# Kernel tuning notes

Hardware: AMD Instinct MI355X
Metric: run time of the kernel (lower is better)

## Reference

```python
import jax, jax.numpy as jnp
import numpy as np

NUM_HEADS = 12
D = 768
HD = D // NUM_HEADS  # 64

def setup_inputs() -> dict:
    key = jax.random.key(0)
    ks = jax.random.split(key, 9)
    s = 0.02
    return {
        "x": jax.random.normal(ks[0], (4, 2048, D), dtype=jnp.float32),
        "QW_w": jax.random.normal(ks[1], (D, D), dtype=jnp.float32) * s,
        "QW_b": jax.random.normal(ks[2], (D,), dtype=jnp.float32) * s,
        "KW_w": jax.random.normal(ks[3], (D, D), dtype=jnp.float32) * s,
        "KW_b": jax.random.normal(ks[4], (D,), dtype=jnp.float32) * s,
        "VW_w": jax.random.normal(ks[5], (D, D), dtype=jnp.float32) * s,
        "VW_b": jax.random.normal(ks[6], (D,), dtype=jnp.float32) * s,
        "OW_w": jax.random.normal(ks[7], (D, D), dtype=jnp.float32) * s,
        "OW_b": jax.random.normal(ks[8], (D,), dtype=jnp.float32) * s,
    }

def reference(x, QW_w, QW_b, KW_w, KW_b, VW_w, VW_b, OW_w, OW_b):
    b, s, _ = x.shape
    # torch nn.Linear: y = x @ W.T + b
    def proj(w, bias):
        y = jnp.einsum('bsd,ed->bse', x, w) + bias
        return y.reshape(b, s, NUM_HEADS, HD).transpose(0, 2, 1, 3)  # [b,h,s,hd]
    q = proj(QW_w, QW_b)
    k = proj(KW_w, KW_b)
    v = proj(VW_w, VW_b)
    scores = jnp.einsum('bhqd,bhkd->bhqk', q, k) / jnp.sqrt(jnp.float32(HD))
    attn = jax.nn.softmax(scores, axis=-1)
    out = jnp.einsum('bhqk,bhkd->bhqd', attn, v)
    out = out.transpose(0, 2, 1, 3).reshape(b, s, NUM_HEADS * HD)
    return jnp.einsum('bsd,ed->bse', out, OW_w) + OW_b
```

## Files before the change

kernel.cpp:

```cpp
#include <hip/hip_runtime.h>
#include <hip/hip_bf16.h>

#define NH  12
#define HD  64
#define DIM 768
#define SEQ 2048
#define NB  4
#define MM  (NB*SEQ)
#define NKB (SEQ/64)
#define N4X (MM*DIM/4)
#define N4W (DIM*DIM/4)

typedef short    v8s  __attribute__((ext_vector_type(8)));
typedef float    v4f  __attribute__((ext_vector_type(4)));
typedef float    v16f __attribute__((ext_vector_type(16)));
typedef unsigned v4u  __attribute__((ext_vector_type(4)));

#if __has_builtin(__builtin_amdgcn_exp2f)
#define EXP2(x) __builtin_amdgcn_exp2f(x)
#else
#define EXP2(x) __builtin_exp2f(x)
#endif

static __device__ __forceinline__ unsigned short f2b(float f) {
    unsigned int u = __float_as_uint(f);
    return (unsigned short)((u + 0x7FFFu + ((u >> 16) & 1u)) >> 16);
}
static __device__ __forceinline__ unsigned cvtpk(float lo, float hi) {
    unsigned r;
    asm("v_cvt_pk_bf16_f32 %0, %1, %2" : "=v"(r) : "v"(lo), "v"(hi));
    return r;
}
static __device__ __forceinline__ void g2l16(const unsigned short* g, unsigned short* l) {
    __builtin_amdgcn_global_load_lds(
        (const __attribute__((address_space(1))) void*)g,
        (__attribute__((address_space(3))) void*)l, 16, 0, 0);
}

__global__ void cast_all(const float* __restrict__ x,
                         const float* __restrict__ qw, const float* __restrict__ kw,
                         const float* __restrict__ vw, const float* __restrict__ ow,
                         unsigned short* __restrict__ xb,
                         unsigned short* __restrict__ wqb, unsigned short* __restrict__ wkb,
                         unsigned short* __restrict__ wvb, unsigned short* __restrict__ wob)
{
    int i = blockIdx.x * blockDim.x + threadIdx.x;
    const float* in; unsigned short* out; int idx;
    if (i < N4X) {
        in = x; out = xb; idx = i;
    } else {
        int j = i - N4X;
        int s = j / N4W;
        idx = j - s * N4W;
        switch (s) {
            case 0:  in = qw; out = wqb; break;
            case 1:  in = kw; out = wkb; break;
            case 2:  in = vw; out = wvb; break;
            default: in = ow; out = wob; break;
        }
    }
    float4 v = reinterpret_cast<const float4*>(in)[idx];
    ushort4 o;
    o.x = f2b(v.x); o.y = f2b(v.y); o.z = f2b(v.z); o.w = f2b(v.w);
    reinterpret_cast<ushort4*>(out)[idx] = o;
}

__global__ __launch_bounds__(256, 3) void gemm_qkv(
    const unsigned short* __restrict__ A,
    const unsigned short* __restrict__ Wq,
    const unsigned short* __restrict__ Wk,
    const unsigned short* __restrict__ Wv,
    const float* __restrict__ bq,
    const float* __restrict__ bk,
    const float* __restrict__ bvp,
    unsigned short* __restrict__ Qb,
    unsigned short* __restrict__ Kfo,
    unsigned short* __restrict__ Vf)
{
    __shared__ __align__(16) unsigned short As[128 * 64];
    __shared__ __align__(16) unsigned short Bs[3][64 * 64];

    const int tid  = threadIdx.x;
    const int w    = tid >> 6, lane = tid & 63;
    const int quad = lane >> 4, l16 = lane & 15;
    const int wm   = w & 1,  wn = w >> 1;
    const int lane8 = lane >> 3, sc = lane & 7;
    const int m0   = blockIdx.x * 128;
    const int h    = blockIdx.y;
    const int n0   = h * 64;

    v4f acc[3][4][2];
    #pragma unroll
    for (int s = 0; s < 3; ++s)
        #pragma unroll
        for (int i = 0; i < 4; ++i)
            #pragma unroll
            for (int j = 0; j < 2; ++j)
                acc[s][i][j] = v4f{0.f, 0.f, 0.f, 0.f};

    for (int kb = 0; kb < DIM; kb += 64) {
        __syncthreads();
        #pragma unroll
        for (int t = 0; t < 4; ++t) {
            int r8 = w * 32 + t * 8;
            int r  = r8 + lane8;
            int gch = sc ^ (r & 7);
            g2l16(&A[(size_t)(m0 + r) * DIM + kb + gch * 8], &As[r8 * 64]);
        }
        #pragma unroll
        for (int u = 0; u < 6; ++u) {
            int G = w * 6 + u;
            int set = G >> 3, rg = G & 7;
            int row = rg * 8 + lane8;
            int gch = sc ^ (row & 7);
            const unsigned short* Wp = (set == 0) ? Wq : (set == 1) ? Wk : Wv;
            g2l16(&Wp[(size_t)(n0 + row) * DIM + kb + gch * 8], &Bs[set][rg * 8 * 64]);
        }
        __syncthreads();
        #pragma unroll
        for (int kk = 0; kk < 64; kk += 32) {
            int chb = kk >> 3;
            v8s a[4];
            #pragma unroll
            for (int i = 0; i < 4; ++i) {
                int m = wm * 64 + i * 16 + l16;
                a[i] = *reinterpret_cast<const v8s*>(
                    &As[m * 64 + (((chb + quad) ^ (m & 7)) << 3)]);
            }
            #pragma unroll
            for (int s = 0; s < 3; ++s) {
                v8s b[2];
                #pragma unroll
                for (int j = 0; j < 2; ++j) {
                    int n = wn * 32 + j * 16 + l16;
                    b[j] = *reinterpret_cast<const v8s*>(
                        &Bs[s][n * 64 + (((chb + quad) ^ (n & 7)) << 3)]);
                }
                #pragma unroll
                for (int i = 0; i < 4; ++i)
                    #pragma unroll
                    for (int j = 0; j < 2; ++j)
                        acc[s][i][j] = __builtin_amdgcn_mfma_f32_16x16x32_bf16(
                            a[i], b[j], acc[s][i][j], 0, 0, 0);
            }
        }
    }

    #pragma unroll
    for (int i = 0; i < 4; ++i) {
        #pragma unroll
        for (int j = 0; j < 2; ++j) {
            int hd = wn * 32 + j * 16 + l16;
            float bias_v = bq[n0 + hd];
            #pragma unroll
            for (int r = 0; r < 4; ++r) {
                int gm = m0 + wm * 64 + i * 16 + quad * 4 + r;
                int bb = gm >> 11, sq = gm & (SEQ - 1);
                Qb[((size_t)(bb * NH + h) * SEQ + sq) * HD + hd] =
                    f2b((acc[0][i][j][r] + bias_v) * 0.1803368801f);
            }
        }
    }
    #pragma unroll
    for (int i = 0; i < 4; ++i) {
        int kh = i >> 1;
        #pragma unroll
        for (int j = 0; j < 2; ++j) {
            int hd = wn * 32 + j * 16 + l16;
            int c  = hd >> 4;
            int half_a = (l16 >> 3) & 1;
            int jj = l16 & 7;
            float bias_v = bk[n0 + hd];
            int gm0 = m0 + wm * 64 + i * 16 + quad * 4;
            int bb = gm0 >> 11, sk = gm0 & (SEQ - 1);
            int t = sk >> 6;
            int l31k = (i & 1) * 16 + quad * 4;
            size_t frag = ((size_t)(bb * NH + h) * NKB + t) * 8 + kh * 4 + c;
            unsigned short* dst = &Kfo[frag * 512 + (half_a * 32 + l31k) * 8 + jj];
            #pragma unroll
            for (int r = 0; r < 4; ++r)
                dst[r * 8] = f2b(acc[1][i][j][r] + bias_v);
        }
    }
    #pragma unroll
    for (int i = 0; i < 4; ++i) {
        #pragma unroll
        for (int j = 0; j < 2; ++j) {
            int hd = wn * 32 + j * 16 + l16;
            int hb = hd >> 5, l31v = hd & 31;
            float bias_v = bvp[n0 + hd];
            int gm0 = m0 + wm * 64 + i * 16 + quad * 4;
            int bb = gm0 >> 11, sk = gm0 & (SEQ - 1);
            int kbi = sk >> 6;
            int halfv = quad >> 1, j0 = (quad & 1) * 4;
            ushort4 pkv;
            pkv.x = f2b(acc[2][i][j][0] + bias_v);
            pkv.y = f2b(acc[2][i][j][1] + bias_v);
            pkv.z = f2b(acc[2][i][j][2] + bias_v);
            pkv.w = f2b(acc[2][i][j][3] + bias_v);
            size_t frag = ((size_t)(bb * NH + h) * NKB + kbi) * 8 + hb * 4 + i;
            *reinterpret_cast<ushort4*>(
                &Vf[frag * 512 + (halfv * 32 + l31v) * 8 + j0]) = pkv;
        }
    }
}

__global__ __launch_bounds__(256, 3) void gemm_o(
    const unsigned short* __restrict__ A,
    const unsigned short* __restrict__ W,
    const float* __restrict__ bias,
    float* __restrict__ out)
{
    __shared__ __align__(16) unsigned short As[128 * 64];
    __shared__ __align__(16) unsigned short Bs[64 * 64];

    const int tid  = threadIdx.x;
    const int w    = tid >> 6, lane = tid & 63;
    const int quad = lane >> 4, l16 = lane & 15;
    const int wm   = w & 1,  wn = w >> 1;
    const int lane8 = lane >> 3, sc = lane & 7;
    const int m0  = blockIdx.x * 128;
    const int n0l = blockIdx.y * 64;

    v4f acc[4][2];
    #pragma unroll
    for (int i = 0; i < 4; ++i)
        #pragma unroll
        for (int j = 0; j < 2; ++j)
            acc[i][j] = v4f{0.f, 0.f, 0.f, 0.f};

    for (int kb = 0; kb < DIM; kb += 64) {
        __syncthreads();
        #pragma unroll
        for (int t = 0; t < 4; ++t) {
            int r8 = w * 32 + t * 8;
            int r  = r8 + lane8;
            int gch = sc ^ (r & 7);
            g2l16(&A[(size_t)(m0 + r) * DIM + kb + gch * 8], &As[r8 * 64]);
        }
        #pragma unroll
        for (int t = 0; t < 2; ++t) {
            int r8 = (w * 2 + t) * 8;
            int r  = r8 + lane8;
            int gch = sc ^ (r & 7);
            g2l16(&W[(size_t)(n0l + r) * DIM + kb + gch * 8], &Bs[r8 * 64]);
        }
        __syncthreads();
        #pragma unroll
        for (int kk = 0; kk < 64; kk += 32) {
            v8s a[4], b[2];
            int chb = kk >> 3;
            #pragma unroll
            for (int i = 0; i < 4; ++i) {
                int m = wm * 64 + i * 16 + l16;
                a[i] = *reinterpret_cast<const v8s*>(
                    &As[m * 64 + (((chb + quad) ^ (m & 7)) << 3)]);
            }
            #pragma unroll
            for (int j = 0; j < 2; ++j) {
                int n = wn * 32 + j * 16 + l16;
                b[j] = *reinterpret_cast<const v8s*>(
                    &Bs[n * 64 + (((chb + quad) ^ (n & 7)) << 3)]);
            }
            #pragma unroll
            for (int i = 0; i < 4; ++i)
                #pragma unroll
                for (int j = 0; j < 2; ++j)
                    acc[i][j] = __builtin_amdgcn_mfma_f32_16x16x32_bf16(a[i], b[j], acc[i][j], 0, 0, 0);
        }
    }

    #pragma unroll
    for (int i = 0; i < 4; ++i) {
        #pragma unroll
        for (int j = 0; j < 2; ++j) {
            int gn = n0l + wn * 32 + j * 16 + l16;
            float bias_v = bias[gn];
            #pragma unroll
            for (int r = 0; r < 4; ++r) {
                int gm = m0 + wm * 64 + i * 16 + quad * 4 + r;
                out[(size_t)gm * DIM + gn] = acc[i][j][r] + bias_v;
            }
        }
    }
}

__global__ __launch_bounds__(256, 3) void attn(
    const unsigned short* __restrict__ Q,
    const unsigned short* __restrict__ Kf,
    const unsigned short* __restrict__ Vf,
    unsigned short* __restrict__ ctx)
{
    __shared__ __align__(16) unsigned short Ks[2][8 * 512];
    __shared__ __align__(16) unsigned short Vs[2][8 * 512];

    const int tid  = threadIdx.x;
    const int w    = tid >> 6, lane = tid & 63;
    const int l31  = lane & 31, half = lane >> 5;

    const int lblk = blockIdx.y * 16 + blockIdx.x;
    const int vblk = (lblk & 7) * 96 + (lblk >> 3);
    const int bh   = vblk >> 4;
    const int b    = bh / NH, h = bh % NH;
    const int q0   = (vblk & 15) * 128 + w * 32;

    const unsigned short* Qp = Q  + ((size_t)bh * SEQ + q0) * HD;
    const unsigned short* Kh = Kf + (size_t)bh * (NKB * 8 * 512);
    const unsigned short* Vh = Vf + (size_t)bh * (NKB * 8 * 512);

    v8s bq[4];
    #pragma unroll
    for (int c = 0; c < 4; ++c)
        bq[c] = *reinterpret_cast<const v8s*>(&Qp[l31 * HD + c * 16 + half * 8]);

    #define STAGE(it_, buf_)                                                   \
        do {                                                                   \
            _Pragma("unroll")                                                  \
            for (int t = 0; t < 2; ++t) {                                      \
                int g = w * 2 + t;                                             \
                g2l16(&Kh[((size_t)(it_) * 8 + g) * 512 + lane * 8],           \
                      &Ks[buf_][g * 512]);                                     \
                g2l16(&Vh[((size_t)(it_) * 8 + g) * 512 + lane * 8],           \
                      &Vs[buf_][g * 512]);                                     \
            }                                                                  \
        } while (0)

    STAGE(0, 0);

    v16f o0a, o0b, o1a, o1b, Z;
    #pragma unroll
    for (int i = 0; i < 16; ++i) {
        o0a[i] = 0.f; o0b[i] = 0.f; o1a[i] = 0.f; o1b[i] = 0.f; Z[i] = 0.f;
    }
    float li = 0.f;

    int cur = 0;
    for (int it = 0; it < NKB; ++it) {
        __syncthreads();
        if (it + 1 < NKB) STAGE(it + 1, cur ^ 1);

        const unsigned short* Kb_ = Ks[cur];
        const unsigned short* Vb_ = Vs[cur];

        v16f s0, s1;
        {
            v8s k0 = *reinterpret_cast<const v8s*>(&Kb_[lane * 8]);
            v8s k1 = *reinterpret_cast<const v8s*>(&Kb_[4 * 512 + lane * 8]);
            s0 = __builtin_amdgcn_mfma_f32_32x32x16_bf16(k0, bq[0], Z, 0, 0, 0);
            s1 = __builtin_amdgcn_mfma_f32_32x32x16_bf16(k1, bq[0], Z, 0, 0, 0);
            #pragma unroll
            for (int c = 1; c < 4; ++c) {
                v8s kc0 = *reinterpret_cast<const v8s*>(&Kb_[(size_t)c * 512 + lane * 8]);
                v8s kc1 = *reinterpret_cast<const v8s*>(&Kb_[(size_t)(4 + c) * 512 + lane * 8]);
                s0 = __builtin_amdgcn_mfma_f32_32x32x16_bf16(kc0, bq[c], s0, 0, 0, 0);
                s1 = __builtin_amdgcn_mfma_f32_32x32x16_bf16(kc1, bq[c], s1, 0, 0, 0);
            }
        }

        unsigned pk[8][2];
        #pragma unroll
        for (int g = 0; g < 4; ++g) {
            float e0 = EXP2(s0[4*g+0]), e1 = EXP2(s0[4*g+1]);
            float e2 = EXP2(s0[4*g+2]), e3 = EXP2(s0[4*g+3]);
            li += (e0 + e1) + (e2 + e3);
            pk[g][0] = cvtpk(e0, e1);
            pk[g][1] = cvtpk(e2, e3);
            float f0 = EXP2(s1[4*g+0]), f1 = EXP2(s1[4*g+1]);
            float f2 = EXP2(s1[4*g+2]), f3 = EXP2(s1[4*g+3]);
            li += (f0 + f1) + (f2 + f3);
            pk[4+g][0] = cvtpk(f0, f1);
            pk[4+g][1] = cvtpk(f2, f3);
        }

        #pragma unroll
        for (int cp = 0; cp < 4; ++cp) {
            unsigned a0 = pk[2*cp][0],   a1 = pk[2*cp][1];
            unsigned b0 = pk[2*cp+1][0], b1 = pk[2*cp+1][1];
            asm("v_permlane32_swap_b32 %0, %1" : "+v"(a0), "+v"(b0));
            asm("v_permlane32_swap_b32 %0, %1" : "+v"(a1), "+v"(b1));
            v4u fw;
            fw.x = a0; fw.y = a1; fw.z = b0; fw.w = b1;
            v8s pf = __builtin_bit_cast(v8s, fw);
            v8s v0 = *reinterpret_cast<const v8s*>(&Vb_[(size_t)cp * 512 + lane * 8]);
            v8s v1 = *reinterpret_cast<const v8s*>(&Vb_[(size_t)(4 + cp) * 512 + lane * 8]);
            if (cp < 2) {
                o0a = __builtin_amdgcn_mfma_f32_32x32x16_bf16(v0, pf, o0a, 0, 0, 0);
                o1a = __builtin_amdgcn_mfma_f32_32x32x16_bf16(v1, pf, o1a, 0, 0, 0);
            } else {
                o0b = __builtin_amdgcn_mfma_f32_32x32x16_bf16(v0, pf, o0b, 0, 0, 0);
                o1b = __builtin_amdgcn_mfma_f32_32x32x16_bf16(v1, pf, o1b, 0, 0, 0);
            }
        }

        cur ^= 1;
    }
    #undef STAGE

    float inv = 1.0f / (li + __shfl_xor(li, 32));

    const int q = q0 + l31;
    size_t base = ((size_t)(b * SEQ + q)) * DIM + h * HD;
    #pragma unroll
    for (int g = 0; g < 4; ++g) {
        int hd0 = 8 * g + 4 * half;
        uint2 u0, u1;
        u0.x = cvtpk((o0a[4*g+0] + o0b[4*g+0]) * inv, (o0a[4*g+1] + o0b[4*g+1]) * inv);
        u0.y = cvtpk((o0a[4*g+2] + o0b[4*g+2]) * inv, (o0a[4*g+3] + o0b[4*g+3]) * inv);
        u1.x = cvtpk((o1a[4*g+0] + o1b[4*g+0]) * inv, (o1a[4*g+1] + o1b[4*g+1]) * inv);
        u1.y = cvtpk((o1a[4*g+2] + o1b[4*g+2]) * inv, (o1a[4*g+3] + o1b[4*g+3]) * inv);
        *reinterpret_cast<uint2*>(&ctx[base + hd0])      = u0;
        *reinterpret_cast<uint2*>(&ctx[base + 32 + hd0]) = u1;
    }
}

extern "C" void kernel_launch(void* const* d_in, const int* in_sizes, int n_in,
                              void* d_out, int out_size, void* d_ws, size_t ws_size,
                              hipStream_t stream) {
    const float* x  = (const float*)d_in[0];
    const float* qw = (const float*)d_in[1]; const float* qb = (const float*)d_in[2];
    const float* kw = (const float*)d_in[3]; const float* kb = (const float*)d_in[4];
    const float* vw = (const float*)d_in[5]; const float* vb = (const float*)d_in[6];
    const float* ow = (const float*)d_in[7]; const float* ob = (const float*)d_in[8];
    float* out = (float*)d_out;

    char* ws = (char*)d_ws;
    size_t off = 0;
    auto alloc = [&](size_t bytes) -> unsigned short* {
        unsigned short* p = (unsigned short*)(ws + off);
        off += (bytes + 255) & ~(size_t)255;
        return p;
    };
    const size_t XB = (size_t)MM * DIM * 2;
    const size_t WB = (size_t)DIM * DIM * 2;
    const size_t QB = (size_t)NB * NH * SEQ * HD * 2;

    unsigned short* xb  = alloc(XB);
    unsigned short* wqb = alloc(WB);
    unsigned short* wkb = alloc(WB);
    unsigned short* wvb = alloc(WB);
    unsigned short* wob = alloc(WB);
    unsigned short* Qb  = alloc(QB);
    unsigned short* Kfb = alloc(QB);
    unsigned short* Vfb = alloc(QB);
    unsigned short* ctx = alloc(XB);

    const int nitems = N4X + 4 * N4W;
    cast_all<<<nitems / 256, 256, 0, stream>>>(
        x, qw, kw, vw, ow, xb, wqb, wkb, wvb, wob);

    gemm_qkv<<<dim3(MM / 128, NH), 256, 0, stream>>>(
        xb, wqb, wkb, wvb, qb, kb, vb, Qb, Kfb, Vfb);

    attn<<<dim3(SEQ / 128, NB * NH), 256, 0, stream>>>(Qb, Kfb, Vfb, ctx);

    gemm_o<<<dim3(MM / 128, DIM / 64), 256, 0, stream>>>(ctx, wob, ob, out);
}
```

Measured before the change: 202.8 us.

## Double-buffer LDS tiles in QKV and output projection GEMMs

Both projection GEMMs now use ping-pong shared-memory buffers. The next K-slice's global-to-LDS loads are issued right after a single barrier and overlap the MFMA work on the current buffer, which removes the second barrier per iteration. The QKV GEMM halves its K step to 32 and uses a new 4-chunk XOR swizzle, so its LDS footprint stays the same. The output GEMM keeps its K step of 64 and doubles its LDS use, which may limit occupancy; the smaller QKV step also means twice as many barriers.

```diff
diff --git a/kernel.cpp b/kernel.cpp
--- a/kernel.cpp
+++ b/kernel.cpp
@@ -77,14 +77,13 @@
     unsigned short* __restrict__ Kfo,
     unsigned short* __restrict__ Vf)
 {
-    __shared__ __align__(16) unsigned short As[128 * 64];
-    __shared__ __align__(16) unsigned short Bs[3][64 * 64];
+    __shared__ __align__(16) unsigned short As[2][128 * 32];
+    __shared__ __align__(16) unsigned short Bs[2][3][64 * 32];
 
     const int tid  = threadIdx.x;
     const int w    = tid >> 6, lane = tid & 63;
     const int quad = lane >> 4, l16 = lane & 15;
     const int wm   = w & 1,  wn = w >> 1;
-    const int lane8 = lane >> 3, sc = lane & 7;
     const int m0   = blockIdx.x * 128;
     const int h    = blockIdx.y;
     const int n0   = h * 64;
@@ -98,53 +97,65 @@
             for (int j = 0; j < 2; ++j)
                 acc[s][i][j] = v4f{0.f, 0.f, 0.f, 0.f};
 
-    for (int kb = 0; kb < DIM; kb += 64) {
+    #define STAGE_QKV(kb_, buf_)                                               \
+        do {                                                                   \
+            _Pragma("unroll")                                                  \
+            for (int t = 0; t < 2; ++t) {                                      \
+                int rb = w * 32 + t * 16;                                      \
+                int r  = rb + (lane >> 2);                                     \
+                int gch = (lane & 3) ^ ((r >> 1) & 3);                         \
+                g2l16(&A[(size_t)(m0 + r) * DIM + (kb_) + gch * 8],            \
+                      &As[buf_][rb * 32]);                                     \
+            }                                                                  \
+            _Pragma("unroll")                                                  \
+            for (int u = 0; u < 3; ++u) {                                      \
+                int G = w * 3 + u;            \
+                int set = G >> 2, rg = G & 3;                                  \
+                int row = rg * 16 + (lane >> 2);                               \
+                int gch = (lane & 3) ^ ((row >> 1) & 3);                       \
+                const unsigned short* Wp = (set == 0) ? Wq                     \
+                                         : (set == 1) ? Wk : Wv;               \
+                g2l16(&Wp[(size_t)(n0 + row) * DIM + (kb_) + gch * 8],         \
+                      &Bs[buf_][set][rg * 16 * 32]);                           \
+            }                                                                  \
+        } while (0)
+
+    STAGE_QKV(0, 0);
+
+    int cur = 0;
+    for (int kb = 0; kb < DIM; kb += 32) {
         __syncthreads();
-        #pragma unroll
-        for (int t = 0; t < 4; ++t) {
-            int r8 = w * 32 + t * 8;
-            int r  = r8 + lane8;
-            int gch = sc ^ (r & 7);
-            g2l16(&A[(size_t)(m0 + r) * DIM + kb + gch * 8], &As[r8 * 64]);
-        }
-        #pragma unroll
-        for (int u = 0; u < 6; ++u) {
-            int G = w * 6 + u;
-            int set = G >> 3, rg = G & 7;
-            int row = rg * 8 + lane8;
-            int gch = sc ^ (row & 7);
-            const unsigned short* Wp = (set == 0) ? Wq : (set == 1) ? Wk : Wv;
-            g2l16(&Wp[(size_t)(n0 + row) * DIM + kb + gch * 8], &Bs[set][rg * 8 * 64]);
-        }
-        __syncthreads();
-        #pragma unroll
-        for (int kk = 0; kk < 64; kk += 32) {
-            int chb = kk >> 3;
-            v8s a[4];
+        if (kb + 32 < DIM) STAGE_QKV(kb + 32, cur ^ 1);
+
+        v8s a[4];
+        #pragma unroll
+        for (int i = 0; i < 4; ++i) {
+            int m = wm * 64 + i * 16 + l16;
+            a[i] = *reinterpret_cast<const v8s*>(
+                &As[cur][m * 32 + ((quad ^ ((m >> 1) & 3)) << 3)]);
+        }
+        #pragma unroll
+        for (int s = 0; s < 3; ++s) {
+            v8s b0, b1;
+            {
+                int n = wn * 32 + l16;
+                b0 = *reinterpret_cast<const v8s*>(
+                    &Bs[cur][s][n * 32 + ((quad ^ ((n >> 1) & 3)) << 3)]);
+                int n2 = n + 16;
+                b1 = *reinterpret_cast<const v8s*>(
+                    &Bs[cur][s][n2 * 32 + ((quad ^ ((n2 >> 1) & 3)) << 3)]);
+            }
             #pragma unroll
             for (int i = 0; i < 4; ++i) {
-                int m = wm * 64 + i * 16 + l16;
-                a[i] = *reinterpret_cast<const v8s*>(
-                    &As[m * 64 + (((chb + quad) ^ (m & 7)) << 3)]);
-            }
-            #pragma unroll
-            for (int s = 0; s < 3; ++s) {
-                v8s b[2];
-                #pragma unroll
-                for (int j = 0; j < 2; ++j) {
-                    int n = wn * 32 + j * 16 + l16;
-                    b[j] = *reinterpret_cast<const v8s*>(
-                        &Bs[s][n * 64 + (((chb + quad) ^ (n & 7)) << 3)]);
-                }
-                #pragma unroll
-                for (int i = 0; i < 4; ++i)
-                    #pragma unroll
-                    for (int j = 0; j < 2; ++j)
-                        acc[s][i][j] = __builtin_amdgcn_mfma_f32_16x16x32_bf16(
-                            a[i], b[j], acc[s][i][j], 0, 0, 0);
-            }
-        }
-    }
+                acc[s][i][0] = __builtin_amdgcn_mfma_f32_16x16x32_bf16(
+                    a[i], b0, acc[s][i][0], 0, 0, 0);
+                acc[s][i][1] = __builtin_amdgcn_mfma_f32_16x16x32_bf16(
+                    a[i], b1, acc[s][i][1], 0, 0, 0);
+            }
+        }
+        cur ^= 1;
+    }
+    #undef STAGE_QKV
 
     #pragma unroll
     for (int i = 0; i < 4; ++i) {
@@ -168,8 +179,8 @@
         for (int j = 0; j < 2; ++j) {
             int hd = wn * 32 + j * 16 + l16;
             int c  = hd >> 4;
+            int jj = l16 & 7;
             int half_a = (l16 >> 3) & 1;
-            int jj = l16 & 7;
             float bias_v = bk[n0 + hd];
             int gm0 = m0 + wm * 64 + i * 16 + quad * 4;
             int bb = gm0 >> 11, sk = gm0 & (SEQ - 1);
@@ -211,8 +222,8 @@
     const float* __restrict__ bias,
     float* __restrict__ out)
 {
-    __shared__ __align__(16) unsigned short As[128 * 64];
-    __shared__ __align__(16) unsigned short Bs[64 * 64];
+    __shared__ __align__(16) unsigned short As[2][128 * 64];
+    __shared__ __align__(16) unsigned short Bs[2][64 * 64];
 
     const int tid  = threadIdx.x;
     const int w    = tid >> 6, lane = tid & 63;
@@ -229,23 +240,33 @@
         for (int j = 0; j < 2; ++j)
             acc[i][j] = v4f{0.f, 0.f, 0.f, 0.f};
 
+    #define STAGE_O(kb_, buf_)                                                 \
+        do {                                                                   \
+            _Pragma("unroll")                                                  \
+            for (int t = 0; t < 4; ++t) {                                      \
+                int r8 = w * 32 + t * 8;                                       \
+                int r  = r8 + lane8;                                           \
+                int gch = sc ^ (r & 7);                                        \
+                g2l16(&A[(size_t)(m0 + r) * DIM + (kb_) + gch * 8],            \
+                      &As[buf_][r8 * 64]);                                     \
+            }                                                                  \
+            _Pragma("unroll")                                                  \
+            for (int t = 0; t < 2; ++t) {                                      \
+                int r8 = (w * 2 + t) * 8;                                      \
+                int r  = r8 + lane8;                                           \
+                int gch = sc ^ (r & 7);                                        \
+                g2l16(&W[(size_t)(n0l + r) * DIM + (kb_) + gch * 8],           \
+                      &Bs[buf_][r8 * 64]);                                     \
+            }                                                                  \
+        } while (0)
+
+    STAGE_O(0, 0);
+
+    int cur = 0;
     for (int kb = 0; kb < DIM; kb += 64) {
         __syncthreads();
-        #pragma unroll
-        for (int t = 0; t < 4; ++t) {
-            int r8 = w * 32 + t * 8;
-            int r  = r8 + lane8;
-            int gch = sc ^ (r & 7);
-            g2l16(&A[(size_t)(m0 + r) * DIM + kb + gch * 8], &As[r8 * 64]);
-        }
-        #pragma unroll
-        for (int t = 0; t < 2; ++t) {
-            int r8 = (w * 2 + t) * 8;
-            int r  = r8 + lane8;
-            int gch = sc ^ (r & 7);
-            g2l16(&W[(size_t)(n0l + r) * DIM + kb + gch * 8], &Bs[r8 * 64]);
-        }
-        __syncthreads();
+        if (kb + 64 < DIM) STAGE_O(kb + 64, cur ^ 1);
+
         #pragma unroll
         for (int kk = 0; kk < 64; kk += 32) {
             v8s a[4], b[2];
@@ -254,13 +275,13 @@
             for (int i = 0; i < 4; ++i) {
                 int m = wm * 64 + i * 16 + l16;
                 a[i] = *reinterpret_cast<const v8s*>(
-                    &As[m * 64 + (((chb + quad) ^ (m & 7)) << 3)]);
+                    &As[cur][m * 64 + (((chb + quad) ^ (m & 7)) << 3)]);
             }
             #pragma unroll
             for (int j = 0; j < 2; ++j) {
                 int n = wn * 32 + j * 16 + l16;
                 b[j] = *reinterpret_cast<const v8s*>(
-                    &Bs[n * 64 + (((chb + quad) ^ (n & 7)) << 3)]);
+                    &Bs[cur][n * 64 + (((chb + quad) ^ (n & 7)) << 3)]);
             }
             #pragma unroll
             for (int i = 0; i < 4; ++i)
@@ -268,7 +289,9 @@
                 for (int j = 0; j < 2; ++j)
                     acc[i][j] = __builtin_amdgcn_mfma_f32_16x16x32_bf16(a[i], b[j], acc[i][j], 0, 0, 0);
         }
-    }
+        cur ^= 1;
+    }
+    #undef STAGE_O
 
     #pragma unroll
     for (int i = 0; i < 4; ++i) {
```

New measurement: 207.0 us. 1.02x slower.
